# Optimization experiments

Hardware: AMD Instinct MI355X
Metric: run time of the kernel (lower is better)

The kernel has to match this reference:

```python
import jax, jax.numpy as jnp
import numpy as np
import math

N, T, D, H = 256, 32, 1024, 1024

def setup_inputs() -> dict:
    key = jax.random.key(0)
    k1, k2, k3, k4, k5 = jax.random.split(key, 5)
    x = jax.random.normal(k1, (N, T, D), dtype=jnp.float32)
    A = jax.random.normal(k2, (N, H, 4, 4), dtype=jnp.float32)
    Wx = jax.random.normal(k3, (D, 4 * H), dtype=jnp.float32) / math.sqrt(D)
    Wh = jax.random.normal(k4, (H, 4 * H), dtype=jnp.float32) / math.sqrt(H)
    Wattn = jax.random.normal(k5, (H, 4 * H), dtype=jnp.float32) / math.sqrt(H)
    b = jnp.zeros((4 * H,), dtype=jnp.float32)
    return {"x": x, "A": A, "Wx": Wx, "Wh": Wh, "Wattn": Wattn, "b": b}

def _forward(x, A, Wx, Wh, Wattn, b):
    Aflat = A.reshape(A.shape[0], A.shape[1], -1)  # (N, H, 16)
    h0 = Aflat.mean(axis=2)  # mean over 4x4 spatial grid -> (N, H)
    c0 = h0
    scale = 1.0 / math.sqrt(Aflat.shape[1])

    def step(carry, xt):
        prev_h, prev_c = carry
        # scaled dot-product attention over 16 spatial locations
        w = jax.nn.softmax(jnp.einsum('nh,nhl->nl', prev_h, Aflat) * scale, axis=-1)  # (N,16)
        attn = jnp.einsum('nhl,nl->nh', Aflat, w)  # (N,H)
        preact = xt @ Wx + prev_h @ Wh + attn @ Wattn + b  # (N,4H)
        ai, af, ao, ag = jnp.split(preact, 4, axis=1)
        i = jax.nn.sigmoid(ai)
        f = jax.nn.sigmoid(af)
        o = jax.nn.sigmoid(ao)
        g = jnp.tanh(ag)
        next_c = f * prev_c + i * g
        next_h = o * jnp.tanh(next_c)
        return (next_h, next_c), next_h

    xT = jnp.swapaxes(x, 0, 1)  # (T, N, D)
    _, hs = jax.lax.scan(step, (h0, c0), xT)
    return jnp.swapaxes(hs, 0, 1)  # (N, T, H)

def reference(x, A, Wx, Wh, Wattn, b):
    return _forward(x, A, Wx, Wh, Wattn, b)
```

## Files before the change

### kernel.cpp

```cpp
#include <hip/hip_runtime.h>

#define N_B 256
#define T_SEQ 32

typedef short short8 __attribute__((ext_vector_type(8)));
typedef float floatx4 __attribute__((ext_vector_type(4)));
typedef unsigned short ushort_t;

__device__ __align__(16) ushort_t g_W2 [(size_t)4096 * 2048];
__device__ __align__(16) ushort_t g_Wat[(size_t)4096 * 1024];
__device__ __align__(16) ushort_t g_xb [(size_t)8192 * 1024];
__device__ __align__(16) ushort_t g_Ab [(size_t)N_B * 16384];
__device__ __align__(16) ushort_t g_At [(size_t)N_B * 16384];
__device__ __align__(16) ushort_t g_P  [(size_t)N_B * 4096 * 16];
__device__ __align__(16) ushort_t g_Hc[2][N_B * 1024];
__device__ __align__(16) float    g_c [N_B * 1024];
__device__ __align__(16) float    g_lg[3][N_B][16];

__device__ __forceinline__ float bf2f(ushort_t u){
    union { unsigned int i; float f; } v; v.i = ((unsigned int)u) << 16; return v.f;
}
__device__ __forceinline__ ushort_t f2bf(float f){
    union { unsigned int i; float f; } v; v.f = f;
    unsigned int i = v.i;
    unsigned int r = (i + 0x7FFFu + ((i >> 16) & 1u)) >> 16;
    return (ushort_t)r;
}
__device__ __forceinline__ float fast_tanh(float x){
    float e = __expf(2.f * x);
    return 1.f - 2.f / (e + 1.f);
}
__device__ __forceinline__ void gload16(const ushort_t* g, ushort_t* l) {
    __builtin_amdgcn_global_load_lds((const __attribute__((address_space(1))) void*)g,
                                     (__attribute__((address_space(3))) void*)l, 16, 0, 0);
}
__device__ __forceinline__ void unp8(uint4 u, float* f) {
    const ushort_t* s = (const ushort_t*)&u;
    #pragma unroll
    for (int i = 0; i < 8; ++i) f[i] = bf2f(s[i]);
}

__global__ __launch_bounds__(128) void cvt_x(const float* __restrict__ x)
{
    int b = blockIdx.x;
    int n = b >> 5, tt = b & 31;
    int tid = threadIdx.x;
    const float* src = x + (size_t)b * 1024 + tid * 8;
    float4 a = *(const float4*)src;
    float4 c = *(const float4*)(src + 4);
    ushort_t r[8];
    r[0]=f2bf(a.x); r[1]=f2bf(a.y); r[2]=f2bf(a.z); r[3]=f2bf(a.w);
    r[4]=f2bf(c.x); r[5]=f2bf(c.y); r[6]=f2bf(c.z); r[7]=f2bf(c.w);
    *(uint4*)(g_xb + (size_t)(tt * 256 + n) * 1024 + tid * 8) = *(const uint4*)r;
}

__global__ __launch_bounds__(256) void cvt_a(const float* __restrict__ A)
{
    int n = blockIdx.x, tid = threadIdx.x;
    int h0 = tid * 4;
    const float* ap = A + (size_t)n * 16384;
    ushort_t tmp[4][16];
    #pragma unroll
    for (int i = 0; i < 4; ++i) {
        const float* row = ap + (size_t)(h0 + i) * 16;
        #pragma unroll
        for (int l = 0; l < 16; ++l) tmp[i][l] = f2bf(row[l]);
        ushort_t* dst = g_Ab + (size_t)n * 16384 + (size_t)(h0 + i) * 16;
        *(uint4*)dst       = *(const uint4*)&tmp[i][0];
        *(uint4*)(dst + 8) = *(const uint4*)&tmp[i][8];
    }
    #pragma unroll
    for (int l = 0; l < 16; ++l) {
        ushort_t pk[4] = { tmp[0][l], tmp[1][l], tmp[2][l], tmp[3][l] };
        *(uint2*)(g_At + (size_t)n * 16384 + (size_t)l * 1024 + h0) = *(const uint2*)pk;
    }
}

__global__ __launch_bounds__(256) void prepack_w2(
    const float* __restrict__ Wh, const float* __restrict__ Wx)
{
    __shared__ ushort_t tile[64][66];
    int k0 = blockIdx.x * 64, j0 = blockIdx.y * 64;
    const float* src = (k0 < 1024) ? Wh : Wx;
    int krel = (k0 < 1024) ? k0 : k0 - 1024;
    int c = threadIdx.x & 63, r4 = threadIdx.x >> 6;
    for (int rr = 0; rr < 64; rr += 4) {
        int r = rr + r4;
        tile[r][c] = f2bf(src[(size_t)(krel + r) * 4096 + j0 + c]);
    }
    __syncthreads();
    for (int rr = 0; rr < 64; rr += 4) {
        int j = rr + r4;
        g_W2[(size_t)(j0 + j) * 2048 + k0 + c] = tile[c][j];
    }
}

__global__ __launch_bounds__(256) void prepack_wat(const float* __restrict__ Wattn)
{
    __shared__ ushort_t tile[64][66];
    int k0 = blockIdx.x * 64, j0 = blockIdx.y * 64;
    int c = threadIdx.x & 63, r4 = threadIdx.x >> 6;
    for (int rr = 0; rr < 64; rr += 4) {
        int r = rr + r4;
        tile[r][c] = f2bf(Wattn[(size_t)(k0 + r) * 4096 + j0 + c]);
    }
    __syncthreads();
    for (int rr = 0; rr < 64; rr += 4) {
        int j = rr + r4;
        g_Wat[(size_t)(j0 + j) * 1024 + k0 + c] = tile[c][j];
    }
}

__global__ __launch_bounds__(256) void zero_lg()
{
    int i = blockIdx.x * 256 + threadIdx.x;
    ((float*)g_lg)[i] = 0.f;
}

__global__ __launch_bounds__(256) void init_hc(const float* __restrict__ A)
{
    __shared__ float l1[16 * 257];
    __shared__ float l2[16 * 16];
    int b = blockIdx.x;
    int n = b >> 2;
    int tid = threadIdx.x;
    int gid = b * 256 + tid;
    const float* ap = A + ((size_t)gid << 4);
    float a[16];
    *(float4*)(a)      = *(const float4*)(ap);
    *(float4*)(a + 4)  = *(const float4*)(ap + 4);
    *(float4*)(a + 8)  = *(const float4*)(ap + 8);
    *(float4*)(a + 12) = *(const float4*)(ap + 12);
    float s = 0.f;
    #pragma unroll
    for (int l = 0; l < 16; ++l) s += a[l];
    s *= (1.0f / 16.0f);
    g_Hc[0][gid] = f2bf(s);
    g_c[gid] = s;
    #pragma unroll
    for (int l = 0; l < 16; ++l) l1[l * 257 + tid] = s * a[l];
    __syncthreads();
    {
        int l = tid >> 4, seg = tid & 15;
        float s2 = 0.f;
        #pragma unroll
        for (int i = 0; i < 16; ++i) s2 += l1[l * 257 + seg * 16 + i];
        l2[l * 16 + seg] = s2;
    }
    __syncthreads();
    if (tid < 16) {
        float lg = 0.f;
        #pragma unroll
        for (int i = 0; i < 16; ++i) lg += l2[tid * 16 + i];
        atomicAdd(&g_lg[0][n][tid], lg);
    }
}

__global__ __launch_bounds__(256) void pw_gemm()
{
    __shared__ __align__(16) char smem[32768];
    ushort_t* lA = (ushort_t*)smem;
    ushort_t* lB = (ushort_t*)(smem + 16384);

    int b = blockIdx.x;
    int xcd = b & 7, q = b >> 3;
    int mb = xcd * 4 + (q & 3), jb = q >> 2;
    int m0 = mb * 128, j0 = jb * 128;
    int tid = threadIdx.x, lane = tid & 63, wv = tid >> 6;
    int wm = wv >> 1, wn = wv & 1;
    int lm = lane & 15, quad = lane >> 4;

    int srow = lane >> 3, sseg = lane & 7;
    const ushort_t* gA = g_At  + (size_t)(m0 + wv * 32 + srow) * 1024 + (sseg ^ srow) * 8;
    const ushort_t* gB = g_Wat + (size_t)(j0 + wv * 32 + srow) * 1024 + (sseg ^ srow) * 8;

    floatx4 acc[4][4] = {};
    for (int kt = 0; kt < 16; ++kt) {
        __syncthreads();
        #pragma unroll
        for (int i = 0; i < 4; ++i) {
            gload16(gA + (size_t)i * 8 * 1024 + kt * 64, lA + (wv * 32 + i * 8) * 64);
            gload16(gB + (size_t)i * 8 * 1024 + kt * 64, lB + (wv * 32 + i * 8) * 64);
        }
        __syncthreads();
        #pragma unroll
        for (int ks = 0; ks < 2; ++ks) {
            short8 af[4], bf[4];
            #pragma unroll
            for (int i = 0; i < 4; ++i) {
                int row = wm*64 + i*16 + lm;
                af[i] = *(const short8*)(lA + row * 64 + (((ks*4 + quad) ^ (row & 7)) * 8));
            }
            #pragma unroll
            for (int j = 0; j < 4; ++j) {
                int row = wn*64 + j*16 + lm;
                bf[j] = *(const short8*)(lB + row * 64 + (((ks*4 + quad) ^ (row & 7)) * 8));
            }
            #pragma unroll
            for (int i = 0; i < 4; ++i)
                #pragma unroll
                for (int j = 0; j < 4; ++j)
                    acc[i][j] = __builtin_amdgcn_mfma_f32_16x16x32_bf16(af[i], bf[j], acc[i][j], 0, 0, 0);
        }
    }

    int n8 = mb * 8;
    #pragma unroll
    for (int i = 0; i < 4; ++i) {
        #pragma unroll
        for (int jf = 0; jf < 4; ++jf) {
            ushort_t pk[4];
            #pragma unroll
            for (int q4 = 0; q4 < 4; ++q4) pk[q4] = f2bf(acc[i][jf][q4]);
            size_t off = ((size_t)(n8 + wm * 4 + i) * 4096
                          + (j0 + wn * 64 + jf * 16 + lm)) * 16 + quad * 4;
            *(uint2*)(g_P + off) = *(const uint2*)pk;
        }
    }
}

__global__ __launch_bounds__(256, 2) void step_gemm(float* __restrict__ out,
                                                    const float* __restrict__ bias, int t)
{
    __shared__ __align__(16) char smem[51200];
    ushort_t* lA0 = (ushort_t*)smem;
    ushort_t* lA1 = (ushort_t*)(smem + 8192);
    ushort_t* lB0 = (ushort_t*)(smem + 16384);
    ushort_t* lB1 = (ushort_t*)(smem + 32768);
    float*    lP  = (float*)smem;
    float*    lq  = (float*)smem;
    float*    lw  = (float*)(smem + 49152);

    const ushort_t* Hin  = g_Hc[t & 1];
    ushort_t*       Hout = g_Hc[(t + 1) & 1];

    int b = blockIdx.x;
    int xcd = b & 7, r = b >> 3;
    int jt = xcd * 8 + (r & 7), nt = r >> 3;
    int n0 = nt * 32, hh0 = jt * 16;
    int tid = threadIdx.x, lane = tid & 63, wv = tid >> 6;
    int lm = lane & 15, quad = lane >> 4;
    int srow = lane >> 4, sseg = lane & 15;

    const ushort_t* hbase = Hin  + (size_t)(n0 + wv * 8 + srow) * 1024;
    const ushort_t* xbase = g_xb + ((size_t)t * 256 + n0 + wv * 8 + srow) * 1024;
    const ushort_t* gB0   = g_W2 + (size_t)(wv * 1024 + hh0 + srow) * 2048;

    #pragma unroll
    for (int i = 0; i < 2; ++i) {
        int rlow = (wv * 8 + i * 4 + srow) & 15;
        gload16(hbase + (size_t)i * 4 * 1024 + (sseg ^ rlow) * 8, lA0 + (wv * 8 + i * 4) * 128);
    }
    #pragma unroll
    for (int i = 0; i < 4; ++i) {
        int rlow = i * 4 + srow;
        gload16(gB0 + (size_t)i * 4 * 2048 + (sseg ^ rlow) * 8, lB0 + (wv * 16 + i * 4) * 128);
    }

    #pragma unroll
    for (int e = 0; e < 2; ++e) {
        int idx = tid + e * 256;
        int nl = idx >> 4, l = idx & 15;
        float v = g_lg[t % 3][n0 + nl][l] * 0.03125f;
        float mx = v;
        mx = fmaxf(mx, __shfl_xor(mx, 1));
        mx = fmaxf(mx, __shfl_xor(mx, 2));
        mx = fmaxf(mx, __shfl_xor(mx, 4));
        mx = fmaxf(mx, __shfl_xor(mx, 8));
        float ex = __expf(v - mx);
        float sm = ex;
        sm += __shfl_xor(sm, 1);
        sm += __shfl_xor(sm, 2);
        sm += __shfl_xor(sm, 4);
        sm += __shfl_xor(sm, 8);
        lw[nl * 16 + l] = ex / sm;
    }
    if (tid < 8) ((float*)g_lg[(t + 2) % 3])[b * 8 + tid] = 0.f;

    floatx4 acc[2][4] = {};
    int segk = wv * 4 + quad;
    for (int it = 0; it < 16; ++it) {
        ushort_t* cA = (it & 1) ? lA1 : lA0;
        ushort_t* cB = (it & 1) ? lB1 : lB0;
        ushort_t* nA = (it & 1) ? lA0 : lA1;
        ushort_t* nB = (it & 1) ? lB0 : lB1;
        if (it < 15) {
            int kk = (it + 1) * 128;
            const ushort_t* aSrc = (kk < 1024) ? (hbase + kk) : (xbase + (kk - 1024));
            #pragma unroll
            for (int i = 0; i < 2; ++i) {
                int rlow = (wv * 8 + i * 4 + srow) & 15;
                gload16(aSrc + (size_t)i * 4 * 1024 + (sseg ^ rlow) * 8,
                        nA + (wv * 8 + i * 4) * 128);
            }
            #pragma unroll
            for (int i = 0; i < 4; ++i) {
                int rlow = i * 4 + srow;
                gload16(gB0 + (size_t)i * 4 * 2048 + kk + (sseg ^ rlow) * 8,
                        nB + (wv * 16 + i * 4) * 128);
            }
            asm volatile("s_waitcnt vmcnt(6)" ::: "memory");
        } else {
            asm volatile("s_waitcnt vmcnt(0)" ::: "memory");
        }
        __builtin_amdgcn_s_barrier();
        short8 af[2], bq[4];
        #pragma unroll
        for (int i = 0; i < 2; ++i)
            af[i] = *(const short8*)(cA + (i * 16 + lm) * 128 + ((segk ^ lm) * 8));
        #pragma unroll
        for (int j = 0; j < 4; ++j)
            bq[j] = *(const short8*)(cB + (j * 16 + lm) * 128 + ((segk ^ lm) * 8));
        #pragma unroll
        for (int i = 0; i < 2; ++i)
            #pragma unroll
            for (int j = 0; j < 4; ++j)
                acc[i][j] = __builtin_amdgcn_mfma_f32_16x16x32_bf16(af[i], bq[j], acc[i][j], 0, 0, 0);
        asm volatile("s_waitcnt lgkmcnt(0)" ::: "memory");
        __builtin_amdgcn_s_barrier();
    }

    float* my = lP + wv * (32 * 68);
    #pragma unroll
    for (int i = 0; i < 2; ++i)
        #pragma unroll
        for (int j = 0; j < 4; ++j)
            #pragma unroll
            for (int q = 0; q < 4; ++q)
                my[(i * 16 + quad * 4 + q) * 68 + j * 16 + lm] = acc[i][j][q];
    __syncthreads();

    float hsave[2];
    #pragma unroll
    for (int e = 0; e < 2; ++e) {
        int idx = tid + e * 256;
        int nl = idx >> 4, hl = idx & 15;
        int base = nl * 68 + hl;
        float s0 = lP[base]      + lP[2176 + base]      + lP[4352 + base]      + lP[6528 + base];
        float s1 = lP[base + 16] + lP[2176 + base + 16] + lP[4352 + base + 16] + lP[6528 + base + 16];
        float s2 = lP[base + 32] + lP[2176 + base + 32] + lP[4352 + base + 32] + lP[6528 + base + 32];
        float s3 = lP[base + 48] + lP[2176 + base + 48] + lP[4352 + base + 48] + lP[6528 + base + 48];
        float wreg[16];
        #pragma unroll
        for (int k = 0; k < 4; ++k)
            *(float4*)(wreg + k * 4) = *(const float4*)(lw + nl * 16 + k * 4);
        int hg = hh0 + hl;
        const ushort_t* pb = g_P + ((size_t)(n0 + nl) * 4096 + hg) * 16;
        float at[4];
        #pragma unroll
        for (int g = 0; g < 4; ++g) {
            const ushort_t* pg = pb + (size_t)g * 1024 * 16;
            float pv[16];
            unp8(*(const uint4*)pg, pv);
            unp8(*(const uint4*)(pg + 8), pv + 8);
            float a = 0.f;
            #pragma unroll
            for (int l = 0; l < 16; ++l) a += wreg[l] * pv[l];
            at[g] = a;
        }
        float ai  = s0 + bias[hg]        + at[0];
        float afv = s1 + bias[1024 + hg] + at[1];
        float ao  = s2 + bias[2048 + hg] + at[2];
        float ag  = s3 + bias[3072 + hg] + at[3];
        float iv = 1.f / (1.f + __expf(-ai));
        float fv = 1.f / (1.f + __expf(-afv));
        float ov = 1.f / (1.f + __expf(-ao));
        float gv = fast_tanh(ag);
        int ng = n0 + nl;
        float cold = g_c[ng * 1024 + hg];
        float cnew = fv * cold + iv * gv;
        float hnew = ov * fast_tanh(cnew);
        g_c[ng * 1024 + hg] = cnew;
        Hout[ng * 1024 + hg] = f2bf(hnew);
        out[(size_t)ng * (T_SEQ * 1024) + (size_t)t * 1024 + hg] = hnew;
        hsave[e] = hnew;
    }

    if (t < T_SEQ - 1) {
        __syncthreads();
        #pragma unroll
        for (int e = 0; e < 2; ++e) {
            int idx = tid + e * 256;
            int nl = idx >> 4, hl = idx & 15;
            const ushort_t* ar = g_Ab + (size_t)(n0 + nl) * 16384 + (size_t)(hh0 + hl) * 16;
            float av[16];
            unp8(*(const uint4*)ar, av);
            unp8(*(const uint4*)(ar + 8), av + 8);
            float hv = hsave[e];
            #pragma unroll
            for (int l = 0; l < 16; ++l)
                lq[(nl * 16 + l) * 17 + hl] = hv * av[l];
        }
        __syncthreads();
        #pragma unroll
        for (int e = 0; e < 2; ++e) {
            int idx = tid + e * 256;
            int nl = idx >> 4, l = idx & 15;
            float s = 0.f;
            #pragma unroll
            for (int k = 0; k < 16; ++k) s += lq[(nl * 16 + l) * 17 + k];
            atomicAdd(&g_lg[(t + 1) % 3][n0 + nl][l], s);
        }
    }
}

extern "C" void kernel_launch(void* const* d_in, const int* in_sizes, int n_in,
                              void* d_out, int out_size, void* d_ws, size_t ws_size,
                              hipStream_t stream) {
    const float* x     = (const float*)d_in[0];
    const float* A     = (const float*)d_in[1];
    const float* Wx    = (const float*)d_in[2];
    const float* Wh    = (const float*)d_in[3];
    const float* Wattn = (const float*)d_in[4];
    const float* bias  = (const float*)d_in[5];
    float* out = (float*)d_out;

    cvt_x<<<8192, 128, 0, stream>>>(x);
    cvt_a<<<256, 256, 0, stream>>>(A);
    prepack_w2<<<dim3(32, 64), 256, 0, stream>>>(Wh, Wx);
    prepack_wat<<<dim3(16, 64), 256, 0, stream>>>(Wattn);
    zero_lg<<<48, 256, 0, stream>>>();
    init_hc<<<1024, 256, 0, stream>>>(A);
    pw_gemm<<<1024, 256, 0, stream>>>();
    for (int t = 0; t < T_SEQ; ++t)
        step_gemm<<<512, 256, 0, stream>>>(out, bias, t);
}
```

Before: 876.8 us.

## Triple-buffer step GEMM loads, prefetch P early, and shard logit atomics

```diff
diff --git a/kernel.cpp b/kernel.cpp
--- a/kernel.cpp
+++ b/kernel.cpp
@@ -15,7 +15,7 @@
 __device__ __align__(16) ushort_t g_P  [(size_t)N_B * 4096 * 16];
 __device__ __align__(16) ushort_t g_Hc[2][N_B * 1024];
 __device__ __align__(16) float    g_c [N_B * 1024];
-__device__ __align__(16) float    g_lg[3][N_B][16];
+__device__ __align__(16) float    g_lg[3][8][N_B][16];
 
 __device__ __forceinline__ float bf2f(ushort_t u){
     union { unsigned int i; float f; } v; v.i = ((unsigned int)u) << 16; return v.f;
@@ -152,7 +152,7 @@
         float lg = 0.f;
         #pragma unroll
         for (int i = 0; i < 16; ++i) lg += l2[tid * 16 + i];
-        atomicAdd(&g_lg[0][n][tid], lg);
+        atomicAdd(&g_lg[0][0][n][tid], lg);
     }
 }
 
@@ -222,14 +222,16 @@
 __global__ __launch_bounds__(256, 2) void step_gemm(float* __restrict__ out,
                                                     const float* __restrict__ bias, int t)
 {
-    __shared__ __align__(16) char smem[51200];
+    __shared__ __align__(16) char smem[75776];
     ushort_t* lA0 = (ushort_t*)smem;
     ushort_t* lA1 = (ushort_t*)(smem + 8192);
-    ushort_t* lB0 = (ushort_t*)(smem + 16384);
-    ushort_t* lB1 = (ushort_t*)(smem + 32768);
+    ushort_t* lA2 = (ushort_t*)(smem + 16384);
+    ushort_t* lB0 = (ushort_t*)(smem + 24576);
+    ushort_t* lB1 = (ushort_t*)(smem + 40960);
+    ushort_t* lB2 = (ushort_t*)(smem + 57344);
     float*    lP  = (float*)smem;
     float*    lq  = (float*)smem;
-    float*    lw  = (float*)(smem + 49152);
+    float*    lw  = (float*)(smem + 73728);
 
     const ushort_t* Hin  = g_Hc[t & 1];
     ushort_t*       Hout = g_Hc[(t + 1) & 1];
@@ -247,21 +249,32 @@
     const ushort_t* gB0   = g_W2 + (size_t)(wv * 1024 + hh0 + srow) * 2048;
 
     #pragma unroll
-    for (int i = 0; i < 2; ++i) {
-        int rlow = (wv * 8 + i * 4 + srow) & 15;
-        gload16(hbase + (size_t)i * 4 * 1024 + (sseg ^ rlow) * 8, lA0 + (wv * 8 + i * 4) * 128);
-    }
-    #pragma unroll
-    for (int i = 0; i < 4; ++i) {
-        int rlow = i * 4 + srow;
-        gload16(gB0 + (size_t)i * 4 * 2048 + (sseg ^ rlow) * 8, lB0 + (wv * 16 + i * 4) * 128);
+    for (int tile = 0; tile < 2; ++tile) {
+        ushort_t* dA = tile ? lA1 : lA0;
+        ushort_t* dB = tile ? lB1 : lB0;
+        int kk = tile * 128;
+        #pragma unroll
+        for (int i = 0; i < 2; ++i) {
+            int rlow = (wv * 8 + i * 4 + srow) & 15;
+            gload16(hbase + (size_t)i * 4 * 1024 + kk + (sseg ^ rlow) * 8,
+                    dA + (wv * 8 + i * 4) * 128);
+        }
+        #pragma unroll
+        for (int i = 0; i < 4; ++i) {
+            int rlow = i * 4 + srow;
+            gload16(gB0 + (size_t)i * 4 * 2048 + kk + (sseg ^ rlow) * 8,
+                    dB + (wv * 16 + i * 4) * 128);
+        }
     }
 
     #pragma unroll
     for (int e = 0; e < 2; ++e) {
         int idx = tid + e * 256;
         int nl = idx >> 4, l = idx & 15;
-        float v = g_lg[t % 3][n0 + nl][l] * 0.03125f;
+        float v = 0.f;
+        #pragma unroll
+        for (int s = 0; s < 8; ++s) v += g_lg[t % 3][s][n0 + nl][l];
+        v *= 0.03125f;
         float mx = v;
         mx = fmaxf(mx, __shfl_xor(mx, 1));
         mx = fmaxf(mx, __shfl_xor(mx, 2));
@@ -275,30 +288,29 @@
         sm += __shfl_xor(sm, 8);
         lw[nl * 16 + l] = ex / sm;
     }
-    if (tid < 8) ((float*)g_lg[(t + 2) % 3])[b * 8 + tid] = 0.f;
+    if (tid < 64) ((float*)g_lg[(t + 2) % 3])[b * 64 + tid] = 0.f;
 
     floatx4 acc[2][4] = {};
     int segk = wv * 4 + quad;
+    ushort_t *cA = lA0, *cB = lB0, *p1A = lA1, *p1B = lB1, *p2A = lA2, *p2B = lB2;
     for (int it = 0; it < 16; ++it) {
-        ushort_t* cA = (it & 1) ? lA1 : lA0;
-        ushort_t* cB = (it & 1) ? lB1 : lB0;
-        ushort_t* nA = (it & 1) ? lA0 : lA1;
-        ushort_t* nB = (it & 1) ? lB0 : lB1;
-        if (it < 15) {
-            int kk = (it + 1) * 128;
+        if (it < 14) {
+            int kk = (it + 2) * 128;
             const ushort_t* aSrc = (kk < 1024) ? (hbase + kk) : (xbase + (kk - 1024));
             #pragma unroll
             for (int i = 0; i < 2; ++i) {
                 int rlow = (wv * 8 + i * 4 + srow) & 15;
                 gload16(aSrc + (size_t)i * 4 * 1024 + (sseg ^ rlow) * 8,
-                        nA + (wv * 8 + i * 4) * 128);
+                        p2A + (wv * 8 + i * 4) * 128);
             }
             #pragma unroll
             for (int i = 0; i < 4; ++i) {
                 int rlow = i * 4 + srow;
                 gload16(gB0 + (size_t)i * 4 * 2048 + kk + (sseg ^ rlow) * 8,
-                        nB + (wv * 16 + i * 4) * 128);
+                        p2B + (wv * 16 + i * 4) * 128);
             }
+            asm volatile("s_waitcnt vmcnt(12)" ::: "memory");
+        } else if (it == 14) {
             asm volatile("s_waitcnt vmcnt(6)" ::: "memory");
         } else {
             asm volatile("s_waitcnt vmcnt(0)" ::: "memory");
@@ -318,6 +330,21 @@
                 acc[i][j] = __builtin_amdgcn_mfma_f32_16x16x32_bf16(af[i], bq[j], acc[i][j], 0, 0, 0);
         asm volatile("s_waitcnt lgkmcnt(0)" ::: "memory");
         __builtin_amdgcn_s_barrier();
+        ushort_t* tA = cA; cA = p1A; p1A = p2A; p2A = tA;
+        ushort_t* tB = cB; cB = p1B; p1B = p2B; p2B = tB;
+    }
+
+    uint4 pld[16];
+    #pragma unroll
+    for (int e = 0; e < 2; ++e) {
+        int idx = tid + e * 256;
+        int nl = idx >> 4, hl = idx & 15;
+        const ushort_t* pb = g_P + ((size_t)(n0 + nl) * 4096 + hh0 + hl) * 16;
+        #pragma unroll
+        for (int g = 0; g < 4; ++g) {
+            pld[e * 8 + g * 2]     = *(const uint4*)(pb + (size_t)g * 16384);
+            pld[e * 8 + g * 2 + 1] = *(const uint4*)(pb + (size_t)g * 16384 + 8);
+        }
     }
 
     float* my = lP + wv * (32 * 68);
@@ -328,7 +355,8 @@
             #pragma unroll
             for (int q = 0; q < 4; ++q)
                 my[(i * 16 + quad * 4 + q) * 68 + j * 16 + lm] = acc[i][j][q];
-    __syncthreads();
+    asm volatile("s_waitcnt lgkmcnt(0)" ::: "memory");
+    __builtin_amdgcn_s_barrier();
 
     float hsave[2];
     #pragma unroll
@@ -344,20 +372,18 @@
         #pragma unroll
         for (int k = 0; k < 4; ++k)
             *(float4*)(wreg + k * 4) = *(const float4*)(lw + nl * 16 + k * 4);
-        int hg = hh0 + hl;
-        const ushort_t* pb = g_P + ((size_t)(n0 + nl) * 4096 + hg) * 16;
         float at[4];
         #pragma unroll
         for (int g = 0; g < 4; ++g) {
-            const ushort_t* pg = pb + (size_t)g * 1024 * 16;
             float pv[16];
-            unp8(*(const uint4*)pg, pv);
-            unp8(*(const uint4*)(pg + 8), pv + 8);
+            unp8(pld[e * 8 + g * 2], pv);
+            unp8(pld[e * 8 + g * 2 + 1], pv + 8);
             float a = 0.f;
             #pragma unroll
             for (int l = 0; l < 16; ++l) a += wreg[l] * pv[l];
             at[g] = a;
         }
+        int hg = hh0 + hl;
         float ai  = s0 + bias[hg]        + at[0];
         float afv = s1 + bias[1024 + hg] + at[1];
         float ao  = s2 + bias[2048 + hg] + at[2];
@@ -399,7 +425,7 @@
             float s = 0.f;
             #pragma unroll
             for (int k = 0; k < 16; ++k) s += lq[(nl * 16 + l) * 17 + k];
-            atomicAdd(&g_lg[(t + 1) % 3][n0 + nl][l], s);
+            atomicAdd(&g_lg[(t + 1) % 3][jt & 7][n0 + nl][l], s);
         }
     }
 }
@@ -419,7 +445,7 @@
     cvt_a<<<256, 256, 0, stream>>>(A);
     prepack_w2<<<dim3(32, 64), 256, 0, stream>>>(Wh, Wx);
     prepack_wat<<<dim3(16, 64), 256, 0, stream>>>(Wattn);
-    zero_lg<<<48, 256, 0, stream>>>();
+    zero_lg<<<384, 256, 0, stream>>>();
     init_hc<<<1024, 256, 0, stream>>>(A);
     pw_gemm<<<1024, 256, 0, stream>>>();
     for (int t = 0; t < T_SEQ; ++t)
```

Result: slower. 902.3 us (+2.9%).

## Fuse per-step launches into one persistent kernel with hierarchical grid barrier

Applied to the files above, without the earlier changes.

```diff
diff --git a/kernel.cpp b/kernel.cpp
--- a/kernel.cpp
+++ b/kernel.cpp
@@ -15,7 +15,9 @@
 __device__ __align__(16) ushort_t g_P  [(size_t)N_B * 4096 * 16];
 __device__ __align__(16) ushort_t g_Hc[2][N_B * 1024];
 __device__ __align__(16) float    g_c [N_B * 1024];
-__device__ __align__(16) float    g_lg[3][N_B][16];
+__device__ __align__(16) float    g_lg[3][8][N_B][16];
+__device__ __align__(128) unsigned int g_sub[16 * 32];
+__device__ unsigned int g_master;
 
 __device__ __forceinline__ float bf2f(ushort_t u){
     union { unsigned int i; float f; } v; v.i = ((unsigned int)u) << 16; return v.f;
@@ -34,10 +36,35 @@
     __builtin_amdgcn_global_load_lds((const __attribute__((address_space(1))) void*)g,
                                      (__attribute__((address_space(3))) void*)l, 16, 0, 0);
 }
+__device__ __forceinline__ void gload16c(const ushort_t* g, ushort_t* l) {
+    __builtin_amdgcn_global_load_lds((const __attribute__((address_space(1))) void*)g,
+                                     (__attribute__((address_space(3))) void*)l, 16, 0, 17);
+}
 __device__ __forceinline__ void unp8(uint4 u, float* f) {
     const ushort_t* s = (const ushort_t*)&u;
     #pragma unroll
     for (int i = 0; i < 8; ++i) f[i] = bf2f(s[i]);
+}
+
+__device__ __forceinline__ void grid_bar(int b, unsigned tsub, unsigned tmaster) {
+    asm volatile("s_waitcnt vmcnt(0)" ::: "memory");
+    __syncthreads();
+    if (threadIdx.x == 0) {
+        __scoped_atomic_thread_fence(__ATOMIC_RELEASE, __MEMORY_SCOPE_DEVICE);
+        __hip_atomic_fetch_add(&g_sub[(b & 15) * 32], 1u,
+                               __ATOMIC_RELAXED, __HIP_MEMORY_SCOPE_AGENT);
+        if (b < 16) {
+            while (__hip_atomic_load(&g_sub[b * 32], __ATOMIC_RELAXED,
+                                     __HIP_MEMORY_SCOPE_AGENT) < tsub)
+                __builtin_amdgcn_s_sleep(2);
+            __hip_atomic_fetch_add(&g_master, 1u,
+                                   __ATOMIC_RELAXED, __HIP_MEMORY_SCOPE_AGENT);
+        }
+        while (__hip_atomic_load(&g_master, __ATOMIC_RELAXED,
+                                 __HIP_MEMORY_SCOPE_AGENT) < tmaster)
+            __builtin_amdgcn_s_sleep(2);
+    }
+    __syncthreads();
 }
 
 __global__ __launch_bounds__(128) void cvt_x(const float* __restrict__ x)
@@ -115,6 +142,8 @@
 {
     int i = blockIdx.x * 256 + threadIdx.x;
     ((float*)g_lg)[i] = 0.f;
+    if (i < 512) g_sub[i] = 0u;
+    if (i == 0) g_master = 0u;
 }
 
 __global__ __launch_bounds__(256) void init_hc(const float* __restrict__ A)
@@ -152,7 +181,7 @@
         float lg = 0.f;
         #pragma unroll
         for (int i = 0; i < 16; ++i) lg += l2[tid * 16 + i];
-        atomicAdd(&g_lg[0][n][tid], lg);
+        atomicAdd(&g_lg[0][0][n][tid], lg);
     }
 }
 
@@ -219,8 +248,8 @@
     }
 }
 
-__global__ __launch_bounds__(256, 2) void step_gemm(float* __restrict__ out,
-                                                    const float* __restrict__ bias, int t)
+__global__ __launch_bounds__(256, 2) void step_loop(float* __restrict__ out,
+                                                    const float* __restrict__ bias)
 {
     __shared__ __align__(16) char smem[51200];
     ushort_t* lA0 = (ushort_t*)smem;
@@ -231,9 +260,6 @@
     float*    lq  = (float*)smem;
     float*    lw  = (float*)(smem + 49152);
 
-    const ushort_t* Hin  = g_Hc[t & 1];
-    ushort_t*       Hout = g_Hc[(t + 1) & 1];
-
     int b = blockIdx.x;
     int xcd = b & 7, r = b >> 3;
     int jt = xcd * 8 + (r & 7), nt = r >> 3;
@@ -242,164 +268,193 @@
     int lm = lane & 15, quad = lane >> 4;
     int srow = lane >> 4, sseg = lane & 15;
 
-    const ushort_t* hbase = Hin  + (size_t)(n0 + wv * 8 + srow) * 1024;
-    const ushort_t* xbase = g_xb + ((size_t)t * 256 + n0 + wv * 8 + srow) * 1024;
-    const ushort_t* gB0   = g_W2 + (size_t)(wv * 1024 + hh0 + srow) * 2048;
-
-    #pragma unroll
-    for (int i = 0; i < 2; ++i) {
-        int rlow = (wv * 8 + i * 4 + srow) & 15;
-        gload16(hbase + (size_t)i * 4 * 1024 + (sseg ^ rlow) * 8, lA0 + (wv * 8 + i * 4) * 128);
-    }
-    #pragma unroll
-    for (int i = 0; i < 4; ++i) {
-        int rlow = i * 4 + srow;
-        gload16(gB0 + (size_t)i * 4 * 2048 + (sseg ^ rlow) * 8, lB0 + (wv * 16 + i * 4) * 128);
-    }
-
-    #pragma unroll
-    for (int e = 0; e < 2; ++e) {
-        int idx = tid + e * 256;
-        int nl = idx >> 4, l = idx & 15;
-        float v = g_lg[t % 3][n0 + nl][l] * 0.03125f;
-        float mx = v;
-        mx = fmaxf(mx, __shfl_xor(mx, 1));
-        mx = fmaxf(mx, __shfl_xor(mx, 2));
-        mx = fmaxf(mx, __shfl_xor(mx, 4));
-        mx = fmaxf(mx, __shfl_xor(mx, 8));
-        float ex = __expf(v - mx);
-        float sm = ex;
-        sm += __shfl_xor(sm, 1);
-        sm += __shfl_xor(sm, 2);
-        sm += __shfl_xor(sm, 4);
-        sm += __shfl_xor(sm, 8);
-        lw[nl * 16 + l] = ex / sm;
-    }
-    if (tid < 8) ((float*)g_lg[(t + 2) % 3])[b * 8 + tid] = 0.f;
-
-    floatx4 acc[2][4] = {};
-    int segk = wv * 4 + quad;
-    for (int it = 0; it < 16; ++it) {
-        ushort_t* cA = (it & 1) ? lA1 : lA0;
-        ushort_t* cB = (it & 1) ? lB1 : lB0;
-        ushort_t* nA = (it & 1) ? lA0 : lA1;
-        ushort_t* nB = (it & 1) ? lB0 : lB1;
-        if (it < 15) {
-            int kk = (it + 1) * 128;
-            const ushort_t* aSrc = (kk < 1024) ? (hbase + kk) : (xbase + (kk - 1024));
-            #pragma unroll
-            for (int i = 0; i < 2; ++i) {
-                int rlow = (wv * 8 + i * 4 + srow) & 15;
-                gload16(aSrc + (size_t)i * 4 * 1024 + (sseg ^ rlow) * 8,
-                        nA + (wv * 8 + i * 4) * 128);
-            }
-            #pragma unroll
-            for (int i = 0; i < 4; ++i) {
-                int rlow = i * 4 + srow;
-                gload16(gB0 + (size_t)i * 4 * 2048 + kk + (sseg ^ rlow) * 8,
-                        nB + (wv * 16 + i * 4) * 128);
-            }
-            asm volatile("s_waitcnt vmcnt(6)" ::: "memory");
-        } else {
-            asm volatile("s_waitcnt vmcnt(0)" ::: "memory");
-        }
-        __builtin_amdgcn_s_barrier();
-        short8 af[2], bq[4];
+    const ushort_t* gB0 = g_W2 + (size_t)(wv * 1024 + hh0 + srow) * 2048;
+
+    float creg[2];
+    {
+        int nlA = tid >> 4, hlA = tid & 15;
+        creg[0] = g_c[(n0 + nlA) * 1024 + hh0 + hlA];
+        creg[1] = g_c[(n0 + 16 + nlA) * 1024 + hh0 + hlA];
+    }
+
+    for (int t = 0; t < T_SEQ; ++t) {
+        if (t) grid_bar(b, 32u * (unsigned)t, 16u * (unsigned)t);
+
+        const ushort_t* Hin  = g_Hc[t & 1];
+        ushort_t*       Hout = g_Hc[(t + 1) & 1];
+        const ushort_t* hbase = Hin  + (size_t)(n0 + wv * 8 + srow) * 1024;
+        const ushort_t* xbase = g_xb + ((size_t)t * 256 + n0 + wv * 8 + srow) * 1024;
+
+        #pragma unroll
+        for (int i = 0; i < 2; ++i) {
+            int rlow = (wv * 8 + i * 4 + srow) & 15;
+            gload16c(hbase + (size_t)i * 4 * 1024 + (sseg ^ rlow) * 8,
+                     lA0 + (wv * 8 + i * 4) * 128);
+        }
+        #pragma unroll
+        for (int i = 0; i < 4; ++i) {
+            int rlow = i * 4 + srow;
+            gload16(gB0 + (size_t)i * 4 * 2048 + (sseg ^ rlow) * 8,
+                    lB0 + (wv * 16 + i * 4) * 128);
+        }
+
+        #pragma unroll
+        for (int e = 0; e < 2; ++e) {
+            int idx = tid + e * 256;
+            int nl = idx >> 4, l = idx & 15;
+            float v = 0.f;
+            #pragma unroll
+            for (int s = 0; s < 8; ++s)
+                v += __hip_atomic_load(&g_lg[t % 3][s][n0 + nl][l],
+                                       __ATOMIC_RELAXED, __HIP_MEMORY_SCOPE_AGENT);
+            v *= 0.03125f;
+            float mx = v;
+            mx = fmaxf(mx, __shfl_xor(mx, 1));
+            mx = fmaxf(mx, __shfl_xor(mx, 2));
+            mx = fmaxf(mx, __shfl_xor(mx, 4));
+            mx = fmaxf(mx, __shfl_xor(mx, 8));
+            float ex = __expf(v - mx);
+            float sm = ex;
+            sm += __shfl_xor(sm, 1);
+            sm += __shfl_xor(sm, 2);
+            sm += __shfl_xor(sm, 4);
+            sm += __shfl_xor(sm, 8);
+            lw[nl * 16 + l] = ex / sm;
+        }
+
+        floatx4 acc[2][4] = {};
+        int segk = wv * 4 + quad;
+        for (int it = 0; it < 16; ++it) {
+            ushort_t* cA = (it & 1) ? lA1 : lA0;
+            ushort_t* cB = (it & 1) ? lB1 : lB0;
+            ushort_t* nA = (it & 1) ? lA0 : lA1;
+            ushort_t* nB = (it & 1) ? lB0 : lB1;
+            if (it < 15) {
+                int kk = (it + 1) * 128;
+                if (kk < 1024) {
+                    #pragma unroll
+                    for (int i = 0; i < 2; ++i) {
+                        int rlow = (wv * 8 + i * 4 + srow) & 15;
+                        gload16c(hbase + (size_t)i * 4 * 1024 + kk + (sseg ^ rlow) * 8,
+                                 nA + (wv * 8 + i * 4) * 128);
+                    }
+                } else {
+                    #pragma unroll
+                    for (int i = 0; i < 2; ++i) {
+                        int rlow = (wv * 8 + i * 4 + srow) & 15;
+                        gload16(xbase + (size_t)i * 4 * 1024 + (kk - 1024) + (sseg ^ rlow) * 8,
+                                nA + (wv * 8 + i * 4) * 128);
+                    }
+                }
+                #pragma unroll
+                for (int i = 0; i < 4; ++i) {
+                    int rlow = i * 4 + srow;
+                    gload16(gB0 + (size_t)i * 4 * 2048 + kk + (sseg ^ rlow) * 8,
+                            nB + (wv * 16 + i * 4) * 128);
+                }
+                asm volatile("s_waitcnt vmcnt(6)" ::: "memory");
+            } else {
+                asm volatile("s_waitcnt vmcnt(0)" ::: "memory");
+            }
+            __builtin_amdgcn_s_barrier();
+            short8 af[2], bq[4];
+            #pragma unroll
+            for (int i = 0; i < 2; ++i)
+                af[i] = *(const short8*)(cA + (i * 16 + lm) * 128 + ((segk ^ lm) * 8));
+            #pragma unroll
+            for (int j = 0; j < 4; ++j)
+                bq[j] = *(const short8*)(cB + (j * 16 + lm) * 128 + ((segk ^ lm) * 8));
+            #pragma unroll
+            for (int i = 0; i < 2; ++i)
+                #pragma unroll
+                for (int j = 0; j < 4; ++j)
+                    acc[i][j] = __builtin_amdgcn_mfma_f32_16x16x32_bf16(af[i], bq[j], acc[i][j], 0, 0, 0);
+            asm volatile("s_waitcnt lgkmcnt(0)" ::: "memory");
+            __builtin_amdgcn_s_barrier();
+        }
+
+        float* my = lP + wv * (32 * 68);
         #pragma unroll
         for (int i = 0; i < 2; ++i)
-            af[i] = *(const short8*)(cA + (i * 16 + lm) * 128 + ((segk ^ lm) * 8));
-        #pragma unroll
-        for (int j = 0; j < 4; ++j)
-            bq[j] = *(const short8*)(cB + (j * 16 + lm) * 128 + ((segk ^ lm) * 8));
-        #pragma unroll
-        for (int i = 0; i < 2; ++i)
             #pragma unroll
             for (int j = 0; j < 4; ++j)
-                acc[i][j] = __builtin_amdgcn_mfma_f32_16x16x32_bf16(af[i], bq[j], acc[i][j], 0, 0, 0);
-        asm volatile("s_waitcnt lgkmcnt(0)" ::: "memory");
-        __builtin_amdgcn_s_barrier();
-    }
-
-    float* my = lP + wv * (32 * 68);
-    #pragma unroll
-    for (int i = 0; i < 2; ++i)
-        #pragma unroll
-        for (int j = 0; j < 4; ++j)
-            #pragma unroll
-            for (int q = 0; q < 4; ++q)
-                my[(i * 16 + quad * 4 + q) * 68 + j * 16 + lm] = acc[i][j][q];
-    __syncthreads();
-
-    float hsave[2];
-    #pragma unroll
-    for (int e = 0; e < 2; ++e) {
-        int idx = tid + e * 256;
-        int nl = idx >> 4, hl = idx & 15;
-        int base = nl * 68 + hl;
-        float s0 = lP[base]      + lP[2176 + base]      + lP[4352 + base]      + lP[6528 + base];
-        float s1 = lP[base + 16] + lP[2176 + base + 16] + lP[4352 + base + 16] + lP[6528 + base + 16];
-        float s2 = lP[base + 32] + lP[2176 + base + 32] + lP[4352 + base + 32] + lP[6528 + base + 32];
-        float s3 = lP[base + 48] + lP[2176 + base + 48] + lP[4352 + base + 48] + lP[6528 + base + 48];
-        float wreg[16];
-        #pragma unroll
-        for (int k = 0; k < 4; ++k)
-            *(float4*)(wreg + k * 4) = *(const float4*)(lw + nl * 16 + k * 4);
-        int hg = hh0 + hl;
-        const ushort_t* pb = g_P + ((size_t)(n0 + nl) * 4096 + hg) * 16;
-        float at[4];
-        #pragma unroll
-        for (int g = 0; g < 4; ++g) {
-            const ushort_t* pg = pb + (size_t)g * 1024 * 16;
-            float pv[16];
-            unp8(*(const uint4*)pg, pv);
-            unp8(*(const uint4*)(pg + 8), pv + 8);
-            float a = 0.f;
-            #pragma unroll
-            for (int l = 0; l < 16; ++l) a += wreg[l] * pv[l];
-            at[g] = a;
-        }
-        float ai  = s0 + bias[hg]        + at[0];
-        float afv = s1 + bias[1024 + hg] + at[1];
-        float ao  = s2 + bias[2048 + hg] + at[2];
-        float ag  = s3 + bias[3072 + hg] + at[3];
-        float iv = 1.f / (1.f + __expf(-ai));
-        float fv = 1.f / (1.f + __expf(-afv));
-        float ov = 1.f / (1.f + __expf(-ao));
-        float gv = fast_tanh(ag);
-        int ng = n0 + nl;
-        float cold = g_c[ng * 1024 + hg];
-        float cnew = fv * cold + iv * gv;
-        float hnew = ov * fast_tanh(cnew);
-        g_c[ng * 1024 + hg] = cnew;
-        Hout[ng * 1024 + hg] = f2bf(hnew);
-        out[(size_t)ng * (T_SEQ * 1024) + (size_t)t * 1024 + hg] = hnew;
-        hsave[e] = hnew;
-    }
-
-    if (t < T_SEQ - 1) {
+                #pragma unroll
+                for (int q = 0; q < 4; ++q)
+                    my[(i * 16 + quad * 4 + q) * 68 + j * 16 + lm] = acc[i][j][q];
         __syncthreads();
+
+        float hsave[2];
         #pragma unroll
         for (int e = 0; e < 2; ++e) {
             int idx = tid + e * 256;
             int nl = idx >> 4, hl = idx & 15;
-            const ushort_t* ar = g_Ab + (size_t)(n0 + nl) * 16384 + (size_t)(hh0 + hl) * 16;
-            float av[16];
-            unp8(*(const uint4*)ar, av);
-            unp8(*(const uint4*)(ar + 8), av + 8);
-            float hv = hsave[e];
-            #pragma unroll
-            for (int l = 0; l < 16; ++l)
-                lq[(nl * 16 + l) * 17 + hl] = hv * av[l];
-        }
-        __syncthreads();
-        #pragma unroll
-        for (int e = 0; e < 2; ++e) {
-            int idx = tid + e * 256;
-            int nl = idx >> 4, l = idx & 15;
-            float s = 0.f;
-            #pragma unroll
-            for (int k = 0; k < 16; ++k) s += lq[(nl * 16 + l) * 17 + k];
-            atomicAdd(&g_lg[(t + 1) % 3][n0 + nl][l], s);
+            int base = nl * 68 + hl;
+            float s0 = lP[base]      + lP[2176 + base]      + lP[4352 + base]      + lP[6528 + base];
+            float s1 = lP[base + 16] + lP[2176 + base + 16] + lP[4352 + base + 16] + lP[6528 + base + 16];
+            float s2 = lP[base + 32] + lP[2176 + base + 32] + lP[4352 + base + 32] + lP[6528 + base + 32];
+            float s3 = lP[base + 48] + lP[2176 + base + 48] + lP[4352 + base + 48] + lP[6528 + base + 48];
+            float wreg[16];
+            #pragma unroll
+            for (int k = 0; k < 4; ++k)
+                *(float4*)(wreg + k * 4) = *(const float4*)(lw + nl * 16 + k * 4);
+            int hg = hh0 + hl;
+            const ushort_t* pb = g_P + ((size_t)(n0 + nl) * 4096 + hg) * 16;
+            float at[4];
+            #pragma unroll
+            for (int g = 0; g < 4; ++g) {
+                const ushort_t* pg = pb + (size_t)g * 16384;
+                float pv[16];
+                unp8(*(const uint4*)pg, pv);
+                unp8(*(const uint4*)(pg + 8), pv + 8);
+                float a = 0.f;
+                #pragma unroll
+                for (int l = 0; l < 16; ++l) a += wreg[l] * pv[l];
+                at[g] = a;
+            }
+            float ai  = s0 + bias[hg]        + at[0];
+            float afv = s1 + bias[1024 + hg] + at[1];
+            float ao  = s2 + bias[2048 + hg] + at[2];
+            float ag  = s3 + bias[3072 + hg] + at[3];
+            float iv = 1.f / (1.f + __expf(-ai));
+            float fv = 1.f / (1.f + __expf(-afv));
+            float ov = 1.f / (1.f + __expf(-ao));
+            float gv = fast_tanh(ag);
+            float cnew = fv * creg[e] + iv * gv;
+            float hnew = ov * fast_tanh(cnew);
+            creg[e] = cnew;
+            int ng = n0 + nl;
+            Hout[ng * 1024 + hg] = f2bf(hnew);
+            out[(size_t)ng * (T_SEQ * 1024) + (size_t)t * 1024 + hg] = hnew;
+            hsave[e] = hnew;
+        }
+
+        if (t < T_SEQ - 1) {
+            __syncthreads();
+            #pragma unroll
+            for (int e = 0; e < 2; ++e) {
+                int idx = tid + e * 256;
+                int nl = idx >> 4, hl = idx & 15;
+                const ushort_t* ar = g_Ab + (size_t)(n0 + nl) * 16384 + (size_t)(hh0 + hl) * 16;
+                float av[16];
+                unp8(*(const uint4*)ar, av);
+                unp8(*(const uint4*)(ar + 8), av + 8);
+                float hv = hsave[e];
+                #pragma unroll
+                for (int l = 0; l < 16; ++l)
+                    lq[(nl * 16 + l) * 17 + hl] = hv * av[l];
+            }
+            __syncthreads();
+            #pragma unroll
+            for (int e = 0; e < 2; ++e) {
+                int idx = tid + e * 256;
+                int nl = idx >> 4, l = idx & 15;
+                float s = 0.f;
+                #pragma unroll
+                for (int k = 0; k < 16; ++k) s += lq[(nl * 16 + l) * 17 + k];
+                atomicAdd(&g_lg[(t + 1) % 3][jt & 7][n0 + nl][l], s);
+            }
+            if (t < T_SEQ - 2 && tid < 64)
+                ((float*)g_lg[(t + 2) % 3])[b * 64 + tid] = 0.f;
         }
     }
 }
@@ -419,9 +474,8 @@
     cvt_a<<<256, 256, 0, stream>>>(A);
     prepack_w2<<<dim3(32, 64), 256, 0, stream>>>(Wh, Wx);
     prepack_wat<<<dim3(16, 64), 256, 0, stream>>>(Wattn);
-    zero_lg<<<48, 256, 0, stream>>>();
+    zero_lg<<<384, 256, 0, stream>>>();
     init_hc<<<1024, 256, 0, stream>>>(A);
     pw_gemm<<<1024, 256, 0, stream>>>();
-    for (int t = 0; t < T_SEQ; ++t)
-        step_gemm<<<512, 256, 0, stream>>>(out, bias, t);
-}
+    step_loop<<<512, 256, 0, stream>>>(out, bias);
+}
```

Measured after the change: 1.259 ms. +43.5%, slower.
